# Kernel optimization log

Measured on AMD Instinct MI355X. Metric: run time of the kernel, lower is better.

The kernel has to match this reference:

```python
import jax, jax.numpy as jnp
import numpy as np

B, L, S, DE, D = 16, 2048, 1024, 512, 256
VOP, NSIL, A, NN = 64, 8, 64, 100000


def setup_inputs() -> dict:
    key = jax.random.key(0)
    ks = jax.random.split(key, 11)
    return {
        "encoded_sentence_tokens": jax.random.normal(ks[0], (B, S, DE), jnp.float32),
        "encoded_stack_nodes": jax.random.normal(ks[1], (NN, D), jnp.float32),
        "silent_embeddings": jax.random.normal(ks[2], (NSIL, D), jnp.float32),
        "op_embedding": jax.random.normal(ks[3], (VOP, D), jnp.float32) * 0.02,
        "w_shift": jax.random.normal(ks[4], (DE, D), jnp.float32) / np.sqrt(DE).astype(np.float32),
        "b_shift": jnp.zeros((D,), jnp.float32),
        "op_tokens": jax.random.randint(ks[5], (B, L), 0, VOP),
        "arg_idx": jax.random.randint(ks[6], (B, L), 0, NSIL + A),
        "shift_idx": jax.random.randint(ks[7], (B, L), 0, S),
        "item_type": jax.random.randint(ks[8], (B, L), 0, 3),
        "avail_nodes": jax.random.randint(ks[9], (B, L, A), 0, NN),
    }


def reference(encoded_sentence_tokens, encoded_stack_nodes, silent_embeddings,
              op_embedding, w_shift, b_shift,
              op_tokens, arg_idx, shift_idx, item_type, avail_nodes):
    # Operation embeddings: [B, L, D]
    emb_ops = op_embedding[op_tokens]

    # Shift-arg embeddings: gather sentence encodings per (b, l), then linear. [B, L, D]
    gathered_sent = jnp.take_along_axis(
        encoded_sentence_tokens, shift_idx[:, :, None], axis=1)  # [B, L, DE]
    emb_shift = jnp.einsum('ble,ed->bld', gathered_sent, w_shift) + b_shift

    # Argument embeddings: choice index < NSIL -> silent embedding, else stack node.
    # Equivalent to concat([silent, available_node_embs], axis=2)[arg_idx] without
    # materializing the [B, L, NSIL+A, D] choice tensor.
    is_silent = arg_idx < NSIL                                    # [B, L]
    silent_sel = silent_embeddings[jnp.clip(arg_idx, 0, NSIL - 1)]  # [B, L, D]
    node_pos = jnp.clip(arg_idx - NSIL, 0, A - 1)                 # [B, L]
    node_ids = jnp.take_along_axis(avail_nodes, node_pos[:, :, None], axis=2)[..., 0]
    node_sel = encoded_stack_nodes[node_ids]                      # [B, L, D]
    emb_args = jnp.where(is_silent[:, :, None], silent_sel, node_sel)

    # combine_embeddings: positional masks align, so it's a 3-way select by type.
    t = item_type[:, :, None]
    result = jnp.where(t == 0, emb_ops,
             jnp.where(t == 1, emb_args,
             jnp.where(t == 2, emb_shift, jnp.zeros_like(emb_ops))))
    return result
```

## Files before the change

kernel.cpp:

```cpp
#include <hip/hip_runtime.h>

#define B_    16
#define L_    2048
#define S_    1024
#define DE_   512
#define D_    256
#define NSIL_ 8
#define A_    64
#define MS_   (B_ * S_)

#define BM 64
#define BN 64
#define BK 32

__global__ __launch_bounds__(256) void srse_gemm(
    const float* __restrict__ sent,
    const float* __restrict__ w,
    const float* __restrict__ bsh,
    float*       __restrict__ P)
{
    __shared__ float As[BK * BM];
    __shared__ float Bs[BK * BN];

    const int t   = threadIdx.x;
    const int bm  = blockIdx.x >> 2;
    const int bn  = blockIdx.x & 3;
    const int gm0 = bm * BM;
    const int gn0 = bn * BN;

    const int tm = (t & 15) * 4;
    const int tn = (t >> 4) * 4;

    float acc[4][4] = {};

    for (int k0 = 0; k0 < DE_; k0 += BK) {
        #pragma unroll
        for (int h = 0; h < 2; ++h) {
            const int idx = t + h * 256;

            const int arow = idx >> 3;
            const int ac   = idx & 7;
            const float4 av = *(const float4*)(sent + (size_t)(gm0 + arow) * DE_ + k0 + ac * 4);
            const int swz = (ac & 3) << 2;
            const int pm  = arow ^ swz;
            As[(ac * 4 + 0) * BM + pm] = av.x;
            As[(ac * 4 + 1) * BM + pm] = av.y;
            As[(ac * 4 + 2) * BM + pm] = av.z;
            As[(ac * 4 + 3) * BM + pm] = av.w;

            const int bkk = idx >> 4;
            const int bc  = idx & 15;
            *(float4*)(Bs + bkk * BN + bc * 4) =
                *(const float4*)(w + (size_t)(k0 + bkk) * D_ + gn0 + bc * 4);
        }
        __syncthreads();

        #pragma unroll
        for (int kk = 0; kk < BK; ++kk) {
            const int swz = ((kk >> 2) & 3) << 2;
            const float4 a4 = *(const float4*)(As + kk * BM + (tm ^ swz));
            const float4 b4 = *(const float4*)(Bs + kk * BN + tn);
            const float a[4] = {a4.x, a4.y, a4.z, a4.w};
            const float b[4] = {b4.x, b4.y, b4.z, b4.w};
            #pragma unroll
            for (int i = 0; i < 4; ++i)
                #pragma unroll
                for (int j = 0; j < 4; ++j)
                    acc[i][j] += a[i] * b[j];
        }
        __syncthreads();
    }

    const float4 bv = *(const float4*)(bsh + gn0 + tn);
    #pragma unroll
    for (int i = 0; i < 4; ++i) {
        float4 o;
        o.x = acc[i][0] + bv.x;
        o.y = acc[i][1] + bv.y;
        o.z = acc[i][2] + bv.z;
        o.w = acc[i][3] + bv.w;
        *(float4*)(P + (size_t)(gm0 + tm + i) * D_ + gn0 + tn) = o;
    }
}

__global__ __launch_bounds__(256) void srse_select(
    const float* __restrict__ P,
    const float* __restrict__ op_emb,
    const float* __restrict__ silent,
    const float* __restrict__ nodes,
    const int*   __restrict__ op_tokens,
    const int*   __restrict__ arg_idx,
    const int*   __restrict__ shift_idx,
    const int*   __restrict__ item_type,
    const int*   __restrict__ avail,
    float*       __restrict__ out)
{
    const int row  = blockIdx.x * 4 + (threadIdx.x >> 6);
    const int lane = threadIdx.x & 63;

    const int t = item_type[row];
    float4 v = {0.0f, 0.0f, 0.0f, 0.0f};

    if (t == 0) {
        v = *(const float4*)(op_emb + (size_t)op_tokens[row] * D_ + lane * 4);
    } else if (t == 1) {
        const int a = arg_idx[row];
        if (a < NSIL_) {
            v = *(const float4*)(silent + (size_t)a * D_ + lane * 4);
        } else {
            int np = a - NSIL_;
            if (np > A_ - 1) np = A_ - 1;
            const int nid = avail[(size_t)row * A_ + np];
            v = *(const float4*)(nodes + (size_t)nid * D_ + lane * 4);
        }
    } else if (t == 2) {
        const int b = row >> 11;
        const int s = shift_idx[row];
        v = *(const float4*)(P + (size_t)(b * S_ + s) * D_ + lane * 4);
    }

    *(float4*)(out + (size_t)row * D_ + lane * 4) = v;
}

extern "C" void kernel_launch(void* const* d_in, const int* in_sizes, int n_in,
                              void* d_out, int out_size, void* d_ws, size_t ws_size,
                              hipStream_t stream) {
    const float* sent      = (const float*)d_in[0];
    const float* nodes     = (const float*)d_in[1];
    const float* silent    = (const float*)d_in[2];
    const float* op_emb    = (const float*)d_in[3];
    const float* w         = (const float*)d_in[4];
    const float* bsh       = (const float*)d_in[5];
    const int*   op_tokens = (const int*)d_in[6];
    const int*   arg_idx   = (const int*)d_in[7];
    const int*   shift_idx = (const int*)d_in[8];
    const int*   item_type = (const int*)d_in[9];
    const int*   avail     = (const int*)d_in[10];
    float*       out       = (float*)d_out;

    float* P = (float*)d_ws;

    srse_gemm<<<(MS_ / BM) * (D_ / BN), 256, 0, stream>>>(sent, w, bsh, P);

    srse_select<<<(B_ * L_) / 4, 256, 0, stream>>>(
        P, op_emb, silent, nodes, op_tokens, arg_idx, shift_idx, item_type,
        avail, out);
}
```

Measured before the change: 241.9 us.

## Use bf16 MFMA for shift GEMM and batch row gathers in select kernel

The fp32 FMA GEMM becomes a bf16 MFMA GEMM with 128x64x64 tiles and swizzled LDS. A new pre-kernel transposes the weight and converts it to bf16, and workgroup IDs are remapped for locality. The select kernel now handles 8 rows per wave and issues all gathers before any store, which raises memory-level parallelism. Rounding to bf16 lowers the precision of the shift embeddings and adds a small extra launch.

Measured after the change: 205.7 us. -15.0%, faster.

```diff
diff --git a/kernel.cpp b/kernel.cpp
--- a/kernel.cpp
+++ b/kernel.cpp
@@ -9,77 +9,113 @@
 #define A_    64
 #define MS_   (B_ * S_)
 
-#define BM 64
+#define BM 128
 #define BN 64
-#define BK 32
+#define BK 64
+
+typedef __attribute__((ext_vector_type(8))) short  short8;
+typedef __attribute__((ext_vector_type(4))) float  f32x4;
+
+__device__ __forceinline__ unsigned short f2bf(float f) {
+    unsigned int x = __builtin_bit_cast(unsigned int, f);
+    x += 0x7fffu + ((x >> 16) & 1u);
+    return (unsigned short)(x >> 16);
+}
+
+__global__ __launch_bounds__(256) void srse_wt(
+    const float* __restrict__ w, unsigned short* __restrict__ wT)
+{
+    const int k = blockIdx.x;
+    const int n = threadIdx.x;
+    wT[n * DE_ + k] = f2bf(w[k * D_ + n]);
+}
 
 __global__ __launch_bounds__(256) void srse_gemm(
-    const float* __restrict__ sent,
-    const float* __restrict__ w,
-    const float* __restrict__ bsh,
-    float*       __restrict__ P)
+    const float*          __restrict__ sent,
+    const unsigned short* __restrict__ wT,
+    const float*          __restrict__ bsh,
+    float*                __restrict__ P)
 {
-    __shared__ float As[BK * BM];
-    __shared__ float Bs[BK * BN];
+    __shared__ alignas(16) unsigned short As[BM * BK];
+    __shared__ alignas(16) unsigned short Bs[BN * BK];
 
-    const int t   = threadIdx.x;
-    const int bm  = blockIdx.x >> 2;
-    const int bn  = blockIdx.x & 3;
-    const int gm0 = bm * BM;
-    const int gn0 = bn * BN;
+    const int nwg  = (MS_ / BM) * (D_ / BN);
+    const int wg   = (blockIdx.x & 7) * (nwg / 8) + (blockIdx.x >> 3);
+    const int bm   = wg >> 2;
+    const int bn   = wg & 3;
+    const int gm0  = bm * BM;
+    const int gn0  = bn * BN;
 
-    const int tm = (t & 15) * 4;
-    const int tn = (t >> 4) * 4;
+    const int t    = threadIdx.x;
+    const int lane = t & 63;
+    const int wid  = t >> 6;
+    const int wm   = wid & 1;
+    const int wn   = wid >> 1;
+    const int fr   = lane & 15;
+    const int fq   = lane >> 4;
 
-    float acc[4][4] = {};
+    f32x4 acc[4][2] = {};
 
     for (int k0 = 0; k0 < DE_; k0 += BK) {
         #pragma unroll
-        for (int h = 0; h < 2; ++h) {
-            const int idx = t + h * 256;
-
-            const int arow = idx >> 3;
-            const int ac   = idx & 7;
-            const float4 av = *(const float4*)(sent + (size_t)(gm0 + arow) * DE_ + k0 + ac * 4);
-            const int swz = (ac & 3) << 2;
-            const int pm  = arow ^ swz;
-            As[(ac * 4 + 0) * BM + pm] = av.x;
-            As[(ac * 4 + 1) * BM + pm] = av.y;
-            As[(ac * 4 + 2) * BM + pm] = av.z;
-            As[(ac * 4 + 3) * BM + pm] = av.w;
-
-            const int bkk = idx >> 4;
-            const int bc  = idx & 15;
-            *(float4*)(Bs + bkk * BN + bc * 4) =
-                *(const float4*)(w + (size_t)(k0 + bkk) * D_ + gn0 + bc * 4);
+        for (int s = 0; s < 4; ++s) {
+            const int id  = s * 256 + t;
+            const int row = id >> 3;
+            const int k8  = id & 7;
+            const float4 a0 = *(const float4*)(sent + (size_t)(gm0 + row) * DE_ + k0 + k8 * 8);
+            const float4 a1 = *(const float4*)(sent + (size_t)(gm0 + row) * DE_ + k0 + k8 * 8 + 4);
+            short8 v;
+            v[0] = f2bf(a0.x); v[1] = f2bf(a0.y); v[2] = f2bf(a0.z); v[3] = f2bf(a0.w);
+            v[4] = f2bf(a1.x); v[5] = f2bf(a1.y); v[6] = f2bf(a1.z); v[7] = f2bf(a1.w);
+            const int widx = (row * BK + k8 * 8) ^ ((row & 7) << 3);
+            *(short8*)(As + widx) = v;
+        }
+        #pragma unroll
+        for (int s = 0; s < 2; ++s) {
+            const int id = s * 256 + t;
+            const int n  = id >> 3;
+            const int k8 = id & 7;
+            short8 v = *(const short8*)(wT + (size_t)(gn0 + n) * DE_ + k0 + k8 * 8);
+            const int widx = (n * BK + k8 * 8) ^ ((n & 7) << 3);
+            *(short8*)(Bs + widx) = v;
         }
         __syncthreads();
 
         #pragma unroll
-        for (int kk = 0; kk < BK; ++kk) {
-            const int swz = ((kk >> 2) & 3) << 2;
-            const float4 a4 = *(const float4*)(As + kk * BM + (tm ^ swz));
-            const float4 b4 = *(const float4*)(Bs + kk * BN + tn);
-            const float a[4] = {a4.x, a4.y, a4.z, a4.w};
-            const float b[4] = {b4.x, b4.y, b4.z, b4.w};
+        for (int ks = 0; ks < 2; ++ks) {
+            short8 af[4], bf[2];
             #pragma unroll
-            for (int i = 0; i < 4; ++i)
+            for (int mf = 0; mf < 4; ++mf) {
+                const int row = wm * 64 + mf * 16 + fr;
+                af[mf] = *(const short8*)(As + ((row * BK + ks * 32 + fq * 8) ^ ((row & 7) << 3)));
+            }
+            #pragma unroll
+            for (int nf = 0; nf < 2; ++nf) {
+                const int n = wn * 32 + nf * 16 + fr;
+                bf[nf] = *(const short8*)(Bs + ((n * BK + ks * 32 + fq * 8) ^ ((n & 7) << 3)));
+            }
+            #pragma unroll
+            for (int mf = 0; mf < 4; ++mf)
                 #pragma unroll
-                for (int j = 0; j < 4; ++j)
-                    acc[i][j] += a[i] * b[j];
+                for (int nf = 0; nf < 2; ++nf)
+                    acc[mf][nf] = __builtin_amdgcn_mfma_f32_16x16x32_bf16(
+                        af[mf], bf[nf], acc[mf][nf], 0, 0, 0);
         }
         __syncthreads();
     }
 
-    const float4 bv = *(const float4*)(bsh + gn0 + tn);
     #pragma unroll
-    for (int i = 0; i < 4; ++i) {
-        float4 o;
-        o.x = acc[i][0] + bv.x;
-        o.y = acc[i][1] + bv.y;
-        o.z = acc[i][2] + bv.z;
-        o.w = acc[i][3] + bv.w;
-        *(float4*)(P + (size_t)(gm0 + tm + i) * D_ + gn0 + tn) = o;
+    for (int nf = 0; nf < 2; ++nf) {
+        const int col = gn0 + wn * 32 + nf * 16 + fr;
+        const float bval = bsh[col];
+        #pragma unroll
+        for (int mf = 0; mf < 4; ++mf) {
+            #pragma unroll
+            for (int r = 0; r < 4; ++r) {
+                const int row = gm0 + wm * 64 + mf * 16 + fq * 4 + r;
+                P[(size_t)row * D_ + col] = acc[mf][nf][r] + bval;
+            }
+        }
     }
 }
 
@@ -95,31 +131,34 @@
     const int*   __restrict__ avail,
     float*       __restrict__ out)
 {
-    const int row  = blockIdx.x * 4 + (threadIdx.x >> 6);
+    const int wid  = threadIdx.x >> 6;
     const int lane = threadIdx.x & 63;
+    const int r0   = blockIdx.x * 32 + wid * 8;
 
-    const int t = item_type[row];
-    float4 v = {0.0f, 0.0f, 0.0f, 0.0f};
-
-    if (t == 0) {
-        v = *(const float4*)(op_emb + (size_t)op_tokens[row] * D_ + lane * 4);
-    } else if (t == 1) {
-        const int a = arg_idx[row];
-        if (a < NSIL_) {
-            v = *(const float4*)(silent + (size_t)a * D_ + lane * 4);
-        } else {
-            int np = a - NSIL_;
-            if (np > A_ - 1) np = A_ - 1;
-            const int nid = avail[(size_t)row * A_ + np];
-            v = *(const float4*)(nodes + (size_t)nid * D_ + lane * 4);
-        }
-    } else if (t == 2) {
-        const int b = row >> 11;
-        const int s = shift_idx[row];
-        v = *(const float4*)(P + (size_t)(b * S_ + s) * D_ + lane * 4);
+    const float* src[8];
+    #pragma unroll
+    for (int i = 0; i < 8; ++i) {
+        const int row = r0 + i;
+        const int tt  = item_type[row];
+        const int a   = arg_idx[row];
+        int np = a - NSIL_;
+        np = np < 0 ? 0 : (np > A_ - 1 ? A_ - 1 : np);
+        const float* s0 = op_emb + (size_t)op_tokens[row] * D_;
+        const float* s1 = (a < NSIL_)
+                          ? silent + (size_t)a * D_
+                          : nodes + (size_t)avail[(size_t)row * A_ + np] * D_;
+        const float* s2 = P + (size_t)((row >> 11) * S_ + shift_idx[row]) * D_;
+        src[i] = (tt == 0) ? s0 : ((tt == 1) ? s1 : s2);
     }
 
-    *(float4*)(out + (size_t)row * D_ + lane * 4) = v;
+    float4 v[8];
+    #pragma unroll
+    for (int i = 0; i < 8; ++i)
+        v[i] = *(const float4*)(src[i] + lane * 4);
+
+    #pragma unroll
+    for (int i = 0; i < 8; ++i)
+        *(float4*)(out + (size_t)(r0 + i) * D_ + lane * 4) = v[i];
 }
 
 extern "C" void kernel_launch(void* const* d_in, const int* in_sizes, int n_in,
@@ -138,11 +177,14 @@
     const int*   avail     = (const int*)d_in[10];
     float*       out       = (float*)d_out;
 
-    float* P = (float*)d_ws;
+    unsigned short* wT = (unsigned short*)d_ws;
+    float*          P  = (float*)((char*)d_ws + D_ * DE_ * sizeof(unsigned short));
 
-    srse_gemm<<<(MS_ / BM) * (D_ / BN), 256, 0, stream>>>(sent, w, bsh, P);
+    srse_wt<<<DE_, 256, 0, stream>>>(w, wT);
 
-    srse_select<<<(B_ * L_) / 4, 256, 0, stream>>>(
+    srse_gemm<<<(MS_ / BM) * (D_ / BN), 256, 0, stream>>>(sent, wT, bsh, P);
+
+    srse_select<<<(B_ * L_) / 32, 256, 0, stream>>>(
         P, op_emb, silent, nodes, op_tokens, arg_idx, shift_idx, item_type,
         avail, out);
 }
```
